# Kernel tuning notes

Measured on AMD Instinct MI355X. Metric: run time of the kernel, lower is better.

## Reference

```python
import jax, jax.numpy as jnp
import numpy as np

KAPPA = 8
TEMP = 200.0
EPS = 1e-15
N, E, D, T = 8192, 131072, 128, 8
P0, P1 = 512, 128
ZI = D - KAPPA  # non-kappa feature dims


def expmap0(u):
    # Poincare ball exp map at origin, c=1
    n = jnp.clip(jnp.linalg.norm(u, axis=-1, keepdims=True), EPS)
    return jnp.tanh(n) * u / n


def logmap0(y):
    # Poincare ball log map at origin, c=1 (clipped for numerical safety)
    n = jnp.clip(jnp.linalg.norm(y, axis=-1, keepdims=True), EPS)
    t = jnp.clip(n, EPS, 1.0 - 1e-5)
    return jnp.arctanh(t) * y / n


def setup_inputs() -> dict:
    key = jax.random.key(0)
    ks = jax.random.split(key, 8)
    g = lambda k, shp: jax.random.normal(k, shp, jnp.float32) / np.float32(np.sqrt(shp[0]))
    return {
        "x": 0.1 * jax.random.normal(ks[0], (N, D), jnp.float32),
        "y": jax.random.normal(ks[1], (T, N), jnp.float32),
        "We0": g(ks[2], (ZI, ZI)), "be0": jnp.zeros((ZI,), jnp.float32),
        "Ws0": g(ks[3], (D, P0)), "bs0": jnp.zeros((P0,), jnp.float32),
        "We1": g(ks[4], (ZI, ZI)), "be1": jnp.zeros((ZI,), jnp.float32),
        "Ws1": g(ks[5], (D, P1)), "bs1": jnp.zeros((P1,), jnp.float32),
        "adj": jax.random.randint(ks[6], (2, E), 0, N),
    }


def _embed_pool(z, agg, We, be, Ws, bs):
    # embed_pool: keep z0, message-pass zi; compute cluster scores s (hyperbolic head)
    z0, zi = z[:, :KAPPA], z[:, KAPPA:]
    zi = agg(zi @ We + be)
    s = expmap0(agg(z @ Ws + bs))
    z = jnp.concatenate([z0, zi], axis=-1)
    S = jax.nn.softmax(logmap0(s) * TEMP, axis=0)  # soft assignment over nodes
    return z, S


def reference(x, y, We0, be0, Ws0, bs0, We1, be1, Ws1, bs1, adj):
    n = x.shape[0]
    # dense adjacency at level 0 (as in the original renorm)
    A0 = jnp.zeros((n, n), x.dtype).at[adj[0], adj[1]].set(1.0)
    # sparse aggregation equivalent to A0 @ h
    agg0 = lambda h: jax.ops.segment_sum(h[adj[1]], adj[0], num_segments=n)

    # ---- level 0 ----
    z, S0 = _embed_pool(x, agg0, We0, be0, Ws0, bs0)
    x1 = jnp.einsum('ij,ik->jk', S0, z)        # [P0, D] pooled features
    y1 = jnp.einsum('ij,ki->kj', S0, y)        # [T, P0] pooled targets
    A1 = jnp.einsum('ji,jk,kl->il', S0, A0, S0)  # [P0, P0] coarsened adjacency
    loss_ent = jax.scipy.special.entr(S0).sum()

    # ---- level 1 (dense weighted adjacency, i.e. dense_to_coo(A1) round trip) ----
    agg1 = lambda h: A1 @ h
    z1, S1 = _embed_pool(x1, agg1, We1, be1, Ws1, bs1)
    x2 = jnp.einsum('ij,ik->jk', S1, z1)       # [P1, D]
    y2 = jnp.einsum('ij,ki->kj', S1, y1)       # [T, P1]
    loss_ent = loss_ent + jax.scipy.special.entr(S1).sum()

    z_r = jnp.concatenate([x, x1, x2], axis=0)   # [N+P0+P1, D]
    y_r = jnp.concatenate([y, y1, y2], axis=-1)  # [T, N+P0+P1]
    return z_r, y_r, loss_ent
```

## Files before the change

### kernel.cpp

```cpp
#include <hip/hip_runtime.h>
#include <hip/hip_bf16.h>

#define NC   8192
#define EC   131072
#define DC   128
#define TC   8
#define P0C  512
#define P1C  128
#define ZIC  120
#define NCAT 248
#define NW0  640
#define TEMPC 200.0f
#define ATANH_MAX 6.1053405f

typedef short short8 __attribute__((ext_vector_type(8)));
typedef float f32x4 __attribute__((ext_vector_type(4)));

__device__ inline unsigned short f2b(float f) {
  union { float f; unsigned u; } x; x.f = f;
  unsigned r = x.u + 0x7FFFu + ((x.u >> 16) & 1u);
  return (unsigned short)(r >> 16);
}
__device__ inline float b2f(unsigned short b) {
  union { unsigned u; float f; } x; x.u = ((unsigned)b) << 16; return x.f;
}

__global__ void k_prep(const float* __restrict__ Ws0, const float* __restrict__ We0,
                       const float* __restrict__ bs0, const float* __restrict__ be0,
                       const float* __restrict__ We1, const float* __restrict__ Ws1,
                       const float* __restrict__ be1, const float* __restrict__ bs1,
                       unsigned short* __restrict__ WcatHi, unsigned short* __restrict__ WcatLo,
                       float* __restrict__ bias0cat,
                       float* __restrict__ Bcat, float* __restrict__ biascat1)
{
  int idx = blockIdx.x * 256 + threadIdx.x;
  const int A = NW0 * DC;
  const int B = A + NW0;
  const int Cc = B + DC * NCAT;
  const int Dd = Cc + NCAT;
  if (idx < A) {
    int n = idx >> 7, k = idx & 127;
    float v;
    if (n < P0C) v = Ws0[(size_t)k * P0C + n];
    else {
      int nn = n - P0C;
      v = (nn < ZIC && k >= 8) ? We0[(size_t)(k - 8) * ZIC + nn] : 0.f;
    }
    unsigned short h = f2b(v);
    WcatHi[idx] = h; WcatLo[idx] = f2b(v - b2f(h));
  } else if (idx < B) {
    int n = idx - A;
    bias0cat[n] = (n < P0C) ? bs0[n] : ((n - P0C) < ZIC ? be0[n - P0C] : 0.f);
  } else if (idx < Cc) {
    int j = idx - B;
    int k = j / NCAT, n = j - k * NCAT;
    float v;
    if (n < ZIC) v = (k >= 8) ? We1[(size_t)(k - 8) * ZIC + n] : 0.f;
    else         v = Ws1[(size_t)k * P1C + (n - ZIC)];
    Bcat[j] = v;
  } else if (idx < Dd) {
    int n = idx - Cc;
    biascat1[n] = (n < ZIC) ? be1[n] : bs1[n - ZIC];
  }
}

__global__ __launch_bounds__(256) void k_mfma_hilo2(
    const unsigned short* __restrict__ Ahi, const unsigned short* __restrict__ Alo,
    const unsigned short* __restrict__ Bhi, const unsigned short* __restrict__ Blo,
    const float* __restrict__ bias, const float* __restrict__ degf,
    float* __restrict__ C0, float* __restrict__ C1)
{
  __shared__ unsigned short Ah[64][136], Al[64][136], Bh[64][136], Bl[64][136];
  const int bm = blockIdx.x * 64, bn = blockIdx.y * 64;
  const int tid = threadIdx.x;
  const int lane = tid & 63, wave = tid >> 6;
  const int lrow = lane & 15, lgrp = lane >> 4;
#pragma unroll
  for (int p = 0; p < 4; ++p) {
    int id = p * 256 + tid;
    int r = id >> 4, c = id & 15;
    *(uint4*)(&Ah[r][c * 8]) = *(const uint4*)(Ahi + (size_t)(bm + r) * 128 + c * 8);
    *(uint4*)(&Al[r][c * 8]) = *(const uint4*)(Alo + (size_t)(bm + r) * 128 + c * 8);
    *(uint4*)(&Bh[r][c * 8]) = *(const uint4*)(Bhi + (size_t)(bn + r) * 128 + c * 8);
    *(uint4*)(&Bl[r][c * 8]) = *(const uint4*)(Blo + (size_t)(bn + r) * 128 + c * 8);
  }
  __syncthreads();
  f32x4 acc[4];
#pragma unroll
  for (int nt = 0; nt < 4; ++nt) acc[nt] = (f32x4){0.f, 0.f, 0.f, 0.f};
#pragma unroll
  for (int kk = 0; kk < 4; ++kk) {
    short8 ah = *(const short8*)(&Ah[wave * 16 + lrow][kk * 32 + lgrp * 8]);
    short8 al = *(const short8*)(&Al[wave * 16 + lrow][kk * 32 + lgrp * 8]);
#pragma unroll
    for (int nt = 0; nt < 4; ++nt) {
      short8 bh = *(const short8*)(&Bh[nt * 16 + lrow][kk * 32 + lgrp * 8]);
      short8 bl = *(const short8*)(&Bl[nt * 16 + lrow][kk * 32 + lgrp * 8]);
      acc[nt] = __builtin_amdgcn_mfma_f32_16x16x32_bf16(ah, bh, acc[nt], 0, 0, 0);
      acc[nt] = __builtin_amdgcn_mfma_f32_16x16x32_bf16(ah, bl, acc[nt], 0, 0, 0);
      acc[nt] = __builtin_amdgcn_mfma_f32_16x16x32_bf16(al, bh, acc[nt], 0, 0, 0);
    }
  }
#pragma unroll
  for (int nt = 0; nt < 4; ++nt) {
    int n = bn + nt * 16 + lrow;
#pragma unroll
    for (int r = 0; r < 4; ++r) {
      int m = bm + wave * 16 + lgrp * 4 + r;
      float v = acc[nt][r] + degf[m] * bias[n];
      if (n < P0C) C0[(size_t)m * P0C + n] = v;
      else if (n - P0C < ZIC) C1[(size_t)m * DC + 8 + (n - P0C)] = v;
    }
  }
}

__global__ __launch_bounds__(256) void k_gemm_nn_part(
    const float* __restrict__ A, int lda,
    const float* __restrict__ B, int ldb,
    float* __restrict__ part,
    int M, int N, int K, int kchunk)
{
  __shared__ float As[16][65];
  __shared__ float Bs[16][65];
  int bm = blockIdx.x * 64, bn = blockIdx.y * 64;
  int z = blockIdx.z;
  int ks = z * kchunk, ke = min(K, ks + kchunk);
  int tid = threadIdx.x;
  int tm = (tid >> 4) << 2, tn = (tid & 15) << 2;
  float acc[4][4] = {};
  for (int k0 = ks; k0 < ke; k0 += 16) {
    for (int i = tid; i < 1024; i += 256) {
      int m = i >> 4, k = i & 15;
      float v = 0.f;
      if (bm + m < M && k0 + k < ke) v = A[(size_t)(bm + m) * lda + k0 + k];
      As[k][m] = v;
    }
    for (int i = tid; i < 1024; i += 256) {
      int k = i >> 6, n = i & 63;
      float v = 0.f;
      if (k0 + k < ke && bn + n < N) v = B[(size_t)(k0 + k) * ldb + bn + n];
      Bs[k][n] = v;
    }
    __syncthreads();
#pragma unroll
    for (int kk = 0; kk < 16; ++kk) {
      float a[4], b[4];
#pragma unroll
      for (int i = 0; i < 4; i++) a[i] = As[kk][tm + i];
#pragma unroll
      for (int j = 0; j < 4; j++) b[j] = Bs[kk][tn + j];
#pragma unroll
      for (int i = 0; i < 4; i++)
#pragma unroll
        for (int j = 0; j < 4; j++) acc[i][j] += a[i] * b[j];
    }
    __syncthreads();
  }
  size_t base = (size_t)z * M * N;
#pragma unroll
  for (int i = 0; i < 4; i++) {
    int m = bm + tm + i; if (m >= M) continue;
#pragma unroll
    for (int j = 0; j < 4; j++) {
      int n = bn + tn + j; if (n >= N) continue;
      part[base + (size_t)m * N + n] = acc[i][j];
    }
  }
}

__global__ void k_reduce_bias(const float* __restrict__ part,
                              const float* __restrict__ bias,
                              float* __restrict__ C, int nparts, int M, int N)
{
  int idx = blockIdx.x * 256 + threadIdx.x;
  if (idx >= M * N) return;
  int n = idx % N;
  float s = 0.f;
  for (int p = 0; p < nparts; ++p) s += part[(size_t)p * M * N + idx];
  if (bias) s += bias[n];
  C[idx] = s;
}

__global__ void k_reduce_stageB(const float* __restrict__ part,
                                const float* __restrict__ x1f,
                                float* __restrict__ z1, float* __restrict__ s1agg,
                                int nparts)
{
  int idx = blockIdx.x * 256 + threadIdx.x;
  const int MN = P0C * NCAT;
  if (idx < MN) {
    int m = idx / NCAT, n = idx - m * NCAT;
    float s = 0.f;
    for (int p = 0; p < nparts; ++p) s += part[(size_t)p * MN + idx];
    if (n < ZIC) z1[(size_t)m * DC + 8 + n] = s;
    else         s1agg[(size_t)m * P1C + (n - ZIC)] = s;
  } else if (idx < MN + P0C * 8) {
    int r = idx - MN; int m = r >> 3, c = r & 7;
    z1[(size_t)m * DC + c] = x1f[(size_t)m * DC + c];
  }
}

__global__ __launch_bounds__(256) void k_gemm_tn(
    const float* __restrict__ A, int lda,
    const float* __restrict__ B, int ldb,
    float* __restrict__ C, int ldc,
    int M, int N, int K, int kchunk)
{
  __shared__ float As[16][65];
  __shared__ float Bs[16][65];
  int bm = blockIdx.x * 64, bn = blockIdx.y * 64;
  int ks = blockIdx.z * kchunk;
  int ke = min(K, ks + kchunk);
  int tid = threadIdx.x;
  int tm = (tid >> 4) << 2, tn = (tid & 15) << 2;
  float acc[4][4] = {};
  for (int k0 = ks; k0 < ke; k0 += 16) {
    for (int i = tid; i < 1024; i += 256) {
      int k = i >> 6, m = i & 63;
      float v = 0.f;
      if (k0 + k < ke && bm + m < M) v = A[(size_t)(k0 + k) * lda + bm + m];
      As[k][m] = v;
    }
    for (int i = tid; i < 1024; i += 256) {
      int k = i >> 6, n = i & 63;
      float v = 0.f;
      if (k0 + k < ke && bn + n < N) v = B[(size_t)(k0 + k) * ldb + bn + n];
      Bs[k][n] = v;
    }
    __syncthreads();
#pragma unroll
    for (int kk = 0; kk < 16; ++kk) {
      float a[4], b[4];
#pragma unroll
      for (int i = 0; i < 4; i++) a[i] = As[kk][tm + i];
#pragma unroll
      for (int j = 0; j < 4; j++) b[j] = Bs[kk][tn + j];
#pragma unroll
      for (int i = 0; i < 4; i++)
#pragma unroll
        for (int j = 0; j < 4; j++) acc[i][j] += a[i] * b[j];
    }
    __syncthreads();
  }
#pragma unroll
  for (int i = 0; i < 4; i++) {
    int m = bm + tm + i; if (m >= M) continue;
#pragma unroll
    for (int j = 0; j < 4; j++) {
      int n = bn + tn + j; if (n >= N) continue;
      atomicAdd(&C[(size_t)m * ldc + n], acc[i][j]);
    }
  }
}

__global__ __launch_bounds__(256) void k_transpose_bf16(
    const float* __restrict__ src, int R, int C,
    unsigned short* __restrict__ dst)
{
  __shared__ float tile[64][65];
  int br = blockIdx.x * 64, bc = blockIdx.y * 64;
  for (int idx = threadIdx.x; idx < 4096; idx += 256) {
    int r = idx >> 6, c = idx & 63;
    tile[r][c] = src[(size_t)(br + r) * C + bc + c];
  }
  __syncthreads();
  for (int idx = threadIdx.x; idx < 4096; idx += 256) {
    int c = idx >> 6, r = idx & 63;
    dst[(size_t)(bc + c) * R + br + r] = f2b(tile[r][c]);
  }
}

__global__ __launch_bounds__(256) void k_transpose_b2b(
    const unsigned short* __restrict__ src, int R, int C,
    unsigned short* __restrict__ dst)
{
  __shared__ unsigned short tile[64][65];
  int br = blockIdx.x * 64, bc = blockIdx.y * 64;
  for (int idx = threadIdx.x; idx < 4096; idx += 256) {
    int r = idx >> 6, c = idx & 63;
    tile[r][c] = src[(size_t)(br + r) * C + bc + c];
  }
  __syncthreads();
  for (int idx = threadIdx.x; idx < 4096; idx += 256) {
    int c = idx >> 6, r = idx & 63;
    dst[(size_t)(bc + c) * R + br + r] = tile[r][c];
  }
}

__global__ __launch_bounds__(256) void k_nt_bf16(
    const unsigned short* __restrict__ At,
    const unsigned short* __restrict__ Bt,
    float* __restrict__ Cpart,
    int M, int N, int K, int kchunk)
{
  __shared__ unsigned short Alds[64][136];
  __shared__ unsigned short Blds[64][136];
  const int bm = blockIdx.x * 64, bn = blockIdx.y * 64;
  const int z = blockIdx.z;
  const int k_beg = z * kchunk, k_end = k_beg + kchunk;
  const int tid = threadIdx.x;
  const int lane = tid & 63, wave = tid >> 6;
  const int lrow = lane & 15, lgrp = lane >> 4;
  f32x4 acc[4];
#pragma unroll
  for (int nt = 0; nt < 4; ++nt) acc[nt] = (f32x4){0.f, 0.f, 0.f, 0.f};

  for (int k0 = k_beg; k0 < k_end; k0 += 128) {
#pragma unroll
    for (int p = 0; p < 4; ++p) {
      int id = p * 256 + tid;
      int r = id >> 4;
      int c = id & 15;
      *(uint4*)(&Alds[r][c * 8]) =
          *(const uint4*)(At + (size_t)(bm + r) * K + k0 + c * 8);
      *(uint4*)(&Blds[r][c * 8]) =
          *(const uint4*)(Bt + (size_t)(bn + r) * K + k0 + c * 8);
    }
    __syncthreads();
#pragma unroll
    for (int kk = 0; kk < 4; ++kk) {
      short8 af = *(const short8*)(&Alds[wave * 16 + lrow][kk * 32 + lgrp * 8]);
#pragma unroll
      for (int nt = 0; nt < 4; ++nt) {
        short8 bf = *(const short8*)(&Blds[nt * 16 + lrow][kk * 32 + lgrp * 8]);
        acc[nt] = __builtin_amdgcn_mfma_f32_16x16x32_bf16(af, bf, acc[nt], 0, 0, 0);
      }
    }
    __syncthreads();
  }
  size_t base = (size_t)z * M * N;
#pragma unroll
  for (int nt = 0; nt < 4; ++nt) {
    int n = bn + nt * 16 + lrow;
#pragma unroll
    for (int r = 0; r < 4; ++r) {
      int m = bm + wave * 16 + lgrp * 4 + r;
      Cpart[base + (size_t)m * N + n] = acc[nt][r];
    }
  }
}

__global__ void k_reduce_parts(const float* __restrict__ part, float* __restrict__ C,
                               int nparts, int sz)
{
  int idx = blockIdx.x * 256 + threadIdx.x;
  if (idx >= sz) return;
  float s = 0.f;
  for (int p = 0; p < nparts; ++p) s += part[(size_t)p * sz + idx];
  C[idx] = s;
}

__global__ void k_count(const int* __restrict__ adj, int* __restrict__ counts)
{
  int e = blockIdx.x * 256 + threadIdx.x;
  if (e < EC) atomicAdd(&counts[adj[e]], 1);
}

__global__ __launch_bounds__(1024) void k_scan(const int* __restrict__ counts,
                                               int* __restrict__ offsets,
                                               float* __restrict__ degf)
{
  __shared__ int tsum[1024];
  int tid = threadIdx.x;
  int base = tid * 8;
  int loc[8]; int s = 0;
#pragma unroll
  for (int i = 0; i < 8; i++) { loc[i] = s; s += counts[base + i]; }
  tsum[tid] = s;
  __syncthreads();
  for (int off = 1; off < 1024; off <<= 1) {
    int v = (tid >= off) ? tsum[tid - off] : 0;
    __syncthreads();
    tsum[tid] += v;
    __syncthreads();
  }
  int excl = (tid == 0) ? 0 : tsum[tid - 1];
#pragma unroll
  for (int i = 0; i < 8; i++) {
    offsets[base + i] = excl + loc[i];
    degf[base + i] = (float)counts[base + i];
  }
  if (tid == 1023) offsets[NC] = tsum[1023];
}

__global__ void k_scatter(const int* __restrict__ adj, const int* __restrict__ offsets,
                          int* __restrict__ fill, int* __restrict__ csr)
{
  int e = blockIdx.x * 256 + threadIdx.x;
  if (e < EC) {
    int d = adj[e], s = adj[EC + e];
    int p = atomicAdd(&fill[d], 1);
    csr[offsets[d] + p] = s;
  }
}

__global__ __launch_bounds__(128) void k_aggX(
    const int* __restrict__ offsets, const int* __restrict__ csr,
    const float* __restrict__ x,
    float* __restrict__ xa, float* __restrict__ z,
    unsigned short* __restrict__ hi, unsigned short* __restrict__ lo)
{
  int j = blockIdx.x;
  int beg = offsets[j], deg = offsets[j + 1] - beg;
  __shared__ int srcs[512];
  bool inl = (deg <= 512);
  if (inl) for (int i = threadIdx.x; i < deg; i += 128) srcs[i] = csr[beg + i];
  __syncthreads();
  int c = threadIdx.x;
  float acc = 0.f;
  if (inl) {
    int i = 0;
    for (; i + 4 <= deg; i += 4) {
      int s0 = srcs[i], s1 = srcs[i+1], s2 = srcs[i+2], s3 = srcs[i+3];
      float v0 = x[(size_t)s0 * DC + c], v1 = x[(size_t)s1 * DC + c];
      float v2 = x[(size_t)s2 * DC + c], v3 = x[(size_t)s3 * DC + c];
      acc += v0; acc += v1; acc += v2; acc += v3;
    }
    for (; i < deg; ++i) acc += x[(size_t)srcs[i] * DC + c];
  } else {
    for (int i = 0; i < deg; ++i) acc += x[(size_t)csr[beg + i] * DC + c];
  }
  xa[(size_t)j * DC + c] = acc;
  unsigned short h = f2b(acc);
  hi[(size_t)j * DC + c] = h;
  lo[(size_t)j * DC + c] = f2b(acc - b2f(h));
  if (c < 8) z[(size_t)j * DC + c] = x[(size_t)j * DC + c];
}

__global__ __launch_bounds__(256) void k_aggM_bf16(
    const int* __restrict__ offsets, const int* __restrict__ csr,
    const unsigned short* __restrict__ S0h, unsigned short* __restrict__ Mbh)
{
  int j = blockIdx.x;
  int beg = offsets[j], deg = offsets[j + 1] - beg;
  __shared__ int srcs[512];
  __shared__ int nv_s;
  bool inl = (deg <= 512);
  if (inl) for (int i = threadIdx.x; i < deg; i += 256) srcs[i] = csr[beg + i];
  __syncthreads();
  if (inl) {
    for (int t = threadIdx.x; t < deg; t += 256) {
      int v = srcs[t];
      for (int u = 0; u < t; ++u)
        if (csr[beg + u] == v) { srcs[t] = -1; break; }
    }
  }
  __syncthreads();
  if (threadIdx.x == 0) {
    int nv = 0;
    if (inl) {
      for (int i = 0; i < deg; i++) if (srcs[i] >= 0) srcs[nv++] = srcs[i];
    }
    nv_s = nv;
  }
  __syncthreads();
  int c2 = threadIdx.x;
  float a0 = 0.f, a1 = 0.f;
  if (inl) {
    int nv = nv_s;
    int i = 0;
    for (; i + 8 <= nv; i += 8) {
      ushort2 v0 = *(const ushort2*)(S0h + (size_t)srcs[i]   * P0C + c2 * 2);
      ushort2 v1 = *(const ushort2*)(S0h + (size_t)srcs[i+1] * P0C + c2 * 2);
      ushort2 v2 = *(const ushort2*)(S0h + (size_t)srcs[i+2] * P0C + c2 * 2);
      ushort2 v3 = *(const ushort2*)(S0h + (size_t)srcs[i+3] * P0C + c2 * 2);
      ushort2 v4 = *(const ushort2*)(S0h + (size_t)srcs[i+4] * P0C + c2 * 2);
      ushort2 v5 = *(const ushort2*)(S0h + (size_t)srcs[i+5] * P0C + c2 * 2);
      ushort2 v6 = *(const ushort2*)(S0h + (size_t)srcs[i+6] * P0C + c2 * 2);
      ushort2 v7 = *(const ushort2*)(S0h + (size_t)srcs[i+7] * P0C + c2 * 2);
      a0 += b2f(v0.x) + b2f(v1.x) + b2f(v2.x) + b2f(v3.x)
          + b2f(v4.x) + b2f(v5.x) + b2f(v6.x) + b2f(v7.x);
      a1 += b2f(v0.y) + b2f(v1.y) + b2f(v2.y) + b2f(v3.y)
          + b2f(v4.y) + b2f(v5.y) + b2f(v6.y) + b2f(v7.y);
    }
    for (; i < nv; ++i) {
      ushort2 v = *(const ushort2*)(S0h + (size_t)srcs[i] * P0C + c2 * 2);
      a0 += b2f(v.x); a1 += b2f(v.y);
    }
  } else {
    for (int i = 0; i < deg; i++) {
      int s = csr[beg + i];
      bool dup = false;
      for (int u = 0; u < i; u++) if (csr[beg + u] == s) { dup = true; break; }
      if (!dup) {
        ushort2 v = *(const ushort2*)(S0h + (size_t)s * P0C + c2 * 2);
        a0 += b2f(v.x); a1 += b2f(v.y);
      }
    }
  }
  ushort2 o2; o2.x = f2b(a0); o2.y = f2b(a1);
  *(ushort2*)(Mbh + (size_t)j * P0C + c2 * 2) = o2;
}

__global__ __launch_bounds__(256) void k_rowscale(const float* __restrict__ U, int cols,
                                                  float* __restrict__ rs)
{
  int r = blockIdx.x;
  const float* row = U + (size_t)r * cols;
  float ss = 0.f;
  for (int c = threadIdx.x; c < cols; c += 256) { float v = row[c]; ss += v * v; }
  for (int off = 32; off > 0; off >>= 1) ss += __shfl_down(ss, off);
  __shared__ float red[4];
  if ((threadIdx.x & 63) == 0) red[threadIdx.x >> 6] = ss;
  __syncthreads();
  if (threadIdx.x == 0) {
    float n = sqrtf(red[0] + red[1] + red[2] + red[3]);
    n = fmaxf(n, 1e-15f);
    rs[r] = TEMPC * fminf(n, ATANH_MAX) / n;
  }
}

__global__ __launch_bounds__(256) void k_smaxA(const float* __restrict__ U,
    const float* __restrict__ rs, float* __restrict__ pm, float* __restrict__ ps,
    int rows, int cols, int rpg)
{
  int lc = threadIdx.x & 63;
  int c = blockIdx.x * 64 + lc;
  int rl = threadIdx.x >> 6;
  int r0 = blockIdx.y * rpg, r1 = min(rows, r0 + rpg);
  float m = -1e30f, s = 0.f;
  for (int r = r0 + rl; r < r1; r += 4) {
    float l = rs[r] * U[(size_t)r * cols + c];
    if (l > m) { s = s * __expf(m - l) + 1.f; m = l; }
    else s += __expf(l - m);
  }
  __shared__ float sm[4][64], sv[4][64];
  sm[rl][lc] = m; sv[rl][lc] = s;
  __syncthreads();
  if (threadIdx.x < 64) {
    float mm = sm[0][threadIdx.x], s2 = sv[0][threadIdx.x];
    for (int q = 1; q < 4; q++) {
      float mq = sm[q][threadIdx.x], sq = sv[q][threadIdx.x];
      float mn = fmaxf(mm, mq);
      s2 = s2 * __expf(mm - mn) + sq * __expf(mq - mn);
      mm = mn;
    }
    pm[(size_t)blockIdx.y * cols + blockIdx.x * 64 + threadIdx.x] = mm;
    ps[(size_t)blockIdx.y * cols + blockIdx.x * 64 + threadIdx.x] = s2;
  }
}

__global__ void k_smaxB(const float* __restrict__ pm, const float* __restrict__ ps,
                        float* __restrict__ colm, float* __restrict__ colsum,
                        int ng, int cols)
{
  int c = blockIdx.x * blockDim.x + threadIdx.x;
  if (c >= cols) return;
  float m = -1e30f, s = 0.f;
  for (int g = 0; g < ng; g++) {
    float mg = pm[(size_t)g * cols + c], sg = ps[(size_t)g * cols + c];
    float mn = fmaxf(m, mg);
    s = s * __expf(m - mn) + sg * __expf(mg - mn);
    m = mn;
  }
  colm[c] = m; colsum[c] = s;
}

__global__ __launch_bounds__(256) void k_smaxC(const float* __restrict__ U,
    const float* __restrict__ rs, const float* __restrict__ colm,
    const float* __restrict__ colsum,
    unsigned short* __restrict__ Sh, unsigned short* __restrict__ ST,
    float* __restrict__ loss, int rows, int cols)
{
  __shared__ unsigned short tile[64][258];
  __shared__ float red[4];
  int lc = threadIdx.x & 63;
  int gc = blockIdx.x * 64 + lc;
  int rl = threadIdx.x >> 6;
  int r0 = blockIdx.y * 256;
  float m = colm[gc], inv = 1.f / colsum[gc];
  float h = 0.f;
  for (int rr = rl; rr < 256; rr += 4) {
    int r = r0 + rr;
    float l = rs[r] * U[(size_t)r * cols + gc];
    float p = __expf(l - m) * inv;
    unsigned short pb = f2b(p);
    Sh[(size_t)r * cols + gc] = pb;
    tile[lc][rr] = pb;
    if (p > 0.f) h -= p * __logf(p);
  }
  for (int off = 32; off > 0; off >>= 1) h += __shfl_down(h, off);
  if ((threadIdx.x & 63) == 0) red[threadIdx.x >> 6] = h;
  __syncthreads();
  if (threadIdx.x == 0) atomicAdd(loss, red[0] + red[1] + red[2] + red[3]);
  int gc0 = blockIdx.x * 64;
  for (int idx = threadIdx.x; idx < 64 * 256; idx += 256) {
    int col = idx >> 8, rr = idx & 255;
    ST[(size_t)(gc0 + col) * rows + r0 + rr] = tile[col][rr];
  }
}

__global__ __launch_bounds__(256) void k_smax_col(const float* __restrict__ U,
    const float* __restrict__ rs, float* __restrict__ S, float* __restrict__ loss,
    int rows, int cols)
{
  int c = blockIdx.x;
  int tid = threadIdx.x;
  int r0 = tid, r1 = tid + 256;
  float v0 = rs[r0] * U[(size_t)r0 * cols + c];
  float v1 = rs[r1] * U[(size_t)r1 * cols + c];
  float m = fmaxf(v0, v1);
  for (int off = 32; off > 0; off >>= 1) m = fmaxf(m, __shfl_xor(m, off));
  __shared__ float red[4];
  if ((tid & 63) == 0) red[tid >> 6] = m;
  __syncthreads();
  m = fmaxf(fmaxf(red[0], red[1]), fmaxf(red[2], red[3]));
  float e0 = __expf(v0 - m), e1 = __expf(v1 - m);
  float s = e0 + e1;
  for (int off = 32; off > 0; off >>= 1) s += __shfl_xor(s, off);
  __syncthreads();
  __shared__ float red2[4];
  if ((tid & 63) == 0) red2[tid >> 6] = s;
  __syncthreads();
  s = red2[0] + red2[1] + red2[2] + red2[3];
  float inv = 1.f / s;
  float p0 = e0 * inv, p1 = e1 * inv;
  S[(size_t)r0 * cols + c] = p0;
  S[(size_t)r1 * cols + c] = p1;
  float h = 0.f;
  if (p0 > 0.f) h -= p0 * __logf(p0);
  if (p1 > 0.f) h -= p1 * __logf(p1);
  for (int off = 32; off > 0; off >>= 1) h += __shfl_xor(h, off);
  __syncthreads();
  __shared__ float red3[4];
  if ((tid & 63) == 0) red3[tid >> 6] = h;
  __syncthreads();
  if (tid == 0) atomicAdd(loss, red3[0] + red3[1] + red3[2] + red3[3]);
}

__global__ __launch_bounds__(256) void k_yS_part(
    const float* __restrict__ Y, int ldy,
    const float* __restrict__ S, int ldS,
    float* __restrict__ part, int K, int C, int kchunk)
{
  int lc = threadIdx.x & 63;
  int c = blockIdx.x * 64 + lc;
  int rl = threadIdx.x >> 6;
  int r0 = blockIdx.y * kchunk, r1 = min(K, r0 + kchunk);
  float acc[8] = {};
  for (int r = r0 + rl; r < r1; r += 4) {
    float sv = S[(size_t)r * ldS + c];
#pragma unroll
    for (int t = 0; t < 8; t++) acc[t] += Y[(size_t)t * ldy + r] * sv;
  }
  __shared__ float red[4][8][64];
#pragma unroll
  for (int t = 0; t < 8; t++) red[rl][t][lc] = acc[t];
  __syncthreads();
  if (rl == 0) {
#pragma unroll
    for (int t = 0; t < 8; t++) {
      float v = red[0][t][lc] + red[1][t][lc] + red[2][t][lc] + red[3][t][lc];
      part[((size_t)blockIdx.y * 8 + t) * C + c] = v;
    }
  }
}

__global__ __launch_bounds__(256) void k_yS_part_b(
    const float* __restrict__ Y, int ldy,
    const unsigned short* __restrict__ S, int ldS,
    float* __restrict__ part, int K, int C, int kchunk)
{
  int lc = threadIdx.x & 63;
  int c = blockIdx.x * 64 + lc;
  int rl = threadIdx.x >> 6;
  int r0 = blockIdx.y * kchunk, r1 = min(K, r0 + kchunk);
  float acc[8] = {};
  for (int r = r0 + rl; r < r1; r += 4) {
    float sv = b2f(S[(size_t)r * ldS + c]);
#pragma unroll
    for (int t = 0; t < 8; t++) acc[t] += Y[(size_t)t * ldy + r] * sv;
  }
  __shared__ float red[4][8][64];
#pragma unroll
  for (int t = 0; t < 8; t++) red[rl][t][lc] = acc[t];
  __syncthreads();
  if (rl == 0) {
#pragma unroll
    for (int t = 0; t < 8; t++) {
      float v = red[0][t][lc] + red[1][t][lc] + red[2][t][lc] + red[3][t][lc];
      part[((size_t)blockIdx.y * 8 + t) * C + c] = v;
    }
  }
}

__global__ void k_yS_red(const float* __restrict__ part, float* __restrict__ outp,
                         int nparts, int sz)
{
  int idx = blockIdx.x * 256 + threadIdx.x;
  if (idx >= sz) return;
  float s = 0.f;
  for (int p = 0; p < nparts; ++p) s += part[(size_t)p * sz + idx];
  outp[idx] = s;
}

__global__ void k_emit_all(const float* __restrict__ x, const float* __restrict__ x1f,
                           const float* __restrict__ x2f, const float* __restrict__ y,
                           const float* __restrict__ y1f, const float* __restrict__ y2f,
                           const float* __restrict__ lossf, float* __restrict__ out,
                           int total)
{
  int idx = blockIdx.x * 256 + threadIdx.x;
  if (idx >= total) return;
  float v;
  if (idx < 1048576) v = x[idx];
  else if (idx < 1114112) v = x1f[idx - 1048576];
  else if (idx < 1130496) v = x2f[idx - 1114112];
  else if (idx < 1201152) {
    int r = idx - 1130496;
    int t = r / 8832, c = r - t * 8832;
    if (c < 8192) v = y[(size_t)t * 8192 + c];
    else if (c < 8704) v = y1f[t * 512 + (c - 8192)];
    else v = y2f[t * 128 + (c - 8704)];
  } else v = lossf[0];
  out[idx] = v;
}

extern "C" void kernel_launch(void* const* d_in, const int* in_sizes, int n_in,
                              void* d_out, int out_size, void* d_ws, size_t ws_size,
                              hipStream_t stream)
{
  (void)in_sizes; (void)n_in; (void)ws_size;
  const float* x   = (const float*)d_in[0];
  const float* y   = (const float*)d_in[1];
  const float* We0 = (const float*)d_in[2];
  const float* be0 = (const float*)d_in[3];
  const float* Ws0 = (const float*)d_in[4];
  const float* bs0 = (const float*)d_in[5];
  const float* We1 = (const float*)d_in[6];
  const float* be1 = (const float*)d_in[7];
  const float* Ws1 = (const float*)d_in[8];
  const float* bs1 = (const float*)d_in[9];
  const int*   adj = (const int*)d_in[10];
  float* out = (float*)d_out;

  float* ws = (float*)d_ws;
  size_t o = 0;
  auto alloc = [&](size_t n) { float* p = ws + o; o += n; return p; };
  float* xa    = alloc((size_t)NC * DC);
  float* sAgg  = alloc((size_t)NC * P0C);
  float* zbuf  = alloc((size_t)NC * DC);
  float* rsc   = alloc(NC);
  float* degf  = alloc(NC);
  float* pm    = alloc(32 * P0C);
  float* ps    = alloc(32 * P0C);
  float* colm  = alloc(P0C);
  float* colsum= alloc(P0C);
  float* s1agg = alloc((size_t)P0C * P1C);
  float* S1    = alloc((size_t)P0C * P1C);
  float* z1    = alloc((size_t)P0C * P1C);
  float* rs1   = alloc(P0C);
  float* x1f   = alloc((size_t)P0C * DC);
  float* A1    = alloc((size_t)P0C * P0C);
  unsigned short* S0T   = (unsigned short*)alloc((size_t)P0C * NC / 2);
  unsigned short* MbT   = (unsigned short*)alloc((size_t)P0C * NC / 2);
  unsigned short* zbufT = (unsigned short*)alloc((size_t)DC * NC / 2);
  unsigned short* S0h   = (unsigned short*)alloc((size_t)NC * P0C / 2);
  unsigned short* xaHi  = (unsigned short*)alloc((size_t)NC * DC / 2);
  unsigned short* xaLo  = (unsigned short*)alloc((size_t)NC * DC / 2);
  unsigned short* WcatHi= (unsigned short*)alloc((size_t)NW0 * DC / 2);
  unsigned short* WcatLo= (unsigned short*)alloc((size_t)NW0 * DC / 2);
  float* bias0cat = alloc(NW0);
  float* Bcat   = alloc((size_t)DC * NCAT);
  float* biascat1= alloc(NCAT);
  float* t1s1   = alloc((size_t)P0C * NCAT);
  float* partSA = alloc((size_t)4 * P0C * NCAT);
  float* partSB = alloc((size_t)8 * P0C * NCAT);
  float* partY1 = alloc((size_t)128 * TC * P0C);
  float* partY2 = alloc((size_t)8 * TC * P1C);
  float* x2f   = alloc((size_t)P1C * DC);
  float* y1f   = alloc((size_t)TC * P0C);
  float* y2f   = alloc((size_t)TC * P1C);
  float* lossf = alloc(1);
  size_t atomicFloats = (size_t)P1C*DC + (size_t)TC*P0C + (size_t)TC*P1C + 1;
  o = (o + 63) & ~(size_t)63;
  int* ibase   = (int*)(ws + o);
  int* counts  = ibase;
  int* fill    = ibase + NC;
  int* offsets = ibase + 2 * NC;
  int* csr     = ibase + 2 * NC + (NC + 1);

  unsigned short* Mbh = (unsigned short*)sAgg;
  float* partsA1 = sAgg + (size_t)2 * 1024 * 1024;
  float* partsX1 = zbuf;

  hipMemsetAsync(x2f, 0, atomicFloats * sizeof(float), stream);
  hipMemsetAsync(counts, 0, 2 * NC * sizeof(int), stream);

  k_count  <<<EC/256, 256, 0, stream>>>(adj, counts);
  k_scan   <<<1, 1024, 0, stream>>>(counts, offsets, degf);
  k_scatter<<<EC/256, 256, 0, stream>>>(adj, offsets, fill, csr);
  k_prep<<<(NW0*DC + NW0 + DC*NCAT + NCAT + 255)/256, 256, 0, stream>>>(
      Ws0, We0, bs0, be0, We1, Ws1, be1, bs1,
      WcatHi, WcatLo, bias0cat, Bcat, biascat1);

  k_aggX<<<NC, 128, 0, stream>>>(offsets, csr, x, xa, zbuf, xaHi, xaLo);
  k_mfma_hilo2<<<dim3(NC/64, NW0/64), 256, 0, stream>>>(xaHi, xaLo, WcatHi, WcatLo,
                                                        bias0cat, degf, sAgg, zbuf);
  k_transpose_bf16<<<dim3(NC/64, DC/64), 256, 0, stream>>>(zbuf, NC, DC, zbufT);

  k_rowscale<<<NC, 256, 0, stream>>>(sAgg, P0C, rsc);
  k_smaxA<<<dim3(P0C/64, 32), 256, 0, stream>>>(sAgg, rsc, pm, ps, NC, P0C, 256);
  k_smaxB<<<P0C/256, 256, 0, stream>>>(pm, ps, colm, colsum, 32, P0C);
  k_smaxC<<<dim3(P0C/64, 32), 256, 0, stream>>>(sAgg, rsc, colm, colsum, S0h, S0T, lossf, NC, P0C);

  k_aggM_bf16<<<NC, 256, 0, stream>>>(offsets, csr, S0h, Mbh);
  k_transpose_b2b<<<dim3(NC/64, P0C/64), 256, 0, stream>>>(Mbh, NC, P0C, MbT);

  k_nt_bf16<<<dim3(P0C/64, P0C/64, 8), 256, 0, stream>>>(S0T, MbT, partsA1, P0C, P0C, NC, 1024);
  k_reduce_parts<<<(P0C*P0C)/256, 256, 0, stream>>>(partsA1, A1, 8, P0C*P0C);
  k_nt_bf16<<<dim3(P0C/64, DC/64, 16), 256, 0, stream>>>(S0T, zbufT, partsX1, P0C, DC, NC, 512);
  k_reduce_parts<<<(P0C*DC)/256, 256, 0, stream>>>(partsX1, x1f, 16, P0C*DC);
  k_yS_part_b<<<dim3(P0C/64, 128), 256, 0, stream>>>(y, NC, S0h, P0C, partY1, NC, P0C, 64);
  k_yS_red<<<(TC*P0C + 255)/256, 256, 0, stream>>>(partY1, y1f, 128, TC*P0C);

  k_gemm_nn_part<<<dim3(P0C/64, 4, 4), 256, 0, stream>>>(x1f, DC, Bcat, NCAT, partSA, P0C, NCAT, DC, 32);
  k_reduce_bias<<<(P0C*NCAT + 255)/256, 256, 0, stream>>>(partSA, biascat1, t1s1, 4, P0C, NCAT);
  k_gemm_nn_part<<<dim3(P0C/64, 4, 8), 256, 0, stream>>>(A1, P0C, t1s1, NCAT, partSB, P0C, NCAT, P0C, 64);
  k_reduce_stageB<<<(P0C*NCAT + P0C*8 + 255)/256, 256, 0, stream>>>(partSB, x1f, z1, s1agg, 8);

  k_rowscale<<<P0C, 256, 0, stream>>>(s1agg, P1C, rs1);
  k_smax_col<<<P1C, 256, 0, stream>>>(s1agg, rs1, S1, lossf, P0C, P1C);
  k_gemm_tn<<<dim3(P1C/64, DC/64, 16), 256, 0, stream>>>(S1, P1C, z1, DC, x2f, DC, P1C, DC, P0C, 32);
  k_yS_part<<<dim3(P1C/64, 8), 256, 0, stream>>>(y1f, P0C, S1, P1C, partY2, P0C, P1C, 64);
  k_yS_red<<<(TC*P1C + 255)/256, 256, 0, stream>>>(partY2, y2f, 8, TC*P1C);

  k_emit_all<<<(out_size + 255)/256, 256, 0, stream>>>(x, x1f, x2f, y, y1f, y2f, lossf, out, out_size);
}
```

Baseline: 304.8 us.

## Fuse row-norm and bf16 transposed z output into level-0 MFMA epilogue

The level-0 MFMA GEMM epilogue now accumulates per-row sums of squares with shuffles and atomics, replacing the separate k_rowscale pass over the 8192x512 score matrix; a small kernel turns these into row scales. It also writes the message-passed z columns directly as transposed bf16, removing the fp32 zbuf and the k_transpose_bf16 kernel, and aggX writes the first 8 columns transposed. The fp32 xa store is dropped, and aggM now uses 512 threads with scalar bf16 loads instead of 256 threads with paired loads. The trade-off is extra atomics, strided 8-byte transposed stores, and a row norm summed in a different order.

```diff
diff --git a/kernel.cpp b/kernel.cpp
--- a/kernel.cpp
+++ b/kernel.cpp
@@ -68,7 +68,8 @@
     const unsigned short* __restrict__ Ahi, const unsigned short* __restrict__ Alo,
     const unsigned short* __restrict__ Bhi, const unsigned short* __restrict__ Blo,
     const float* __restrict__ bias, const float* __restrict__ degf,
-    float* __restrict__ C0, float* __restrict__ C1)
+    float* __restrict__ C0, unsigned short* __restrict__ zT,
+    float* __restrict__ rs_ss)
 {
   __shared__ unsigned short Ah[64][136], Al[64][136], Bh[64][136], Bl[64][136];
   const int bm = blockIdx.x * 64, bn = blockIdx.y * 64;
@@ -101,17 +102,58 @@
       acc[nt] = __builtin_amdgcn_mfma_f32_16x16x32_bf16(al, bh, acc[nt], 0, 0, 0);
     }
   }
-#pragma unroll
-  for (int nt = 0; nt < 4; ++nt) {
-    int n = bn + nt * 16 + lrow;
+  if (bn < P0C) {
+    float pr[4] = {0.f, 0.f, 0.f, 0.f};
+#pragma unroll
+    for (int nt = 0; nt < 4; ++nt) {
+      int n = bn + nt * 16 + lrow;
+#pragma unroll
+      for (int r = 0; r < 4; ++r) {
+        int m = bm + wave * 16 + lgrp * 4 + r;
+        float v = acc[nt][r] + degf[m] * bias[n];
+        C0[(size_t)m * P0C + n] = v;
+        pr[r] += v * v;
+      }
+    }
 #pragma unroll
     for (int r = 0; r < 4; ++r) {
-      int m = bm + wave * 16 + lgrp * 4 + r;
-      float v = acc[nt][r] + degf[m] * bias[n];
-      if (n < P0C) C0[(size_t)m * P0C + n] = v;
-      else if (n - P0C < ZIC) C1[(size_t)m * DC + 8 + (n - P0C)] = v;
-    }
-  }
+      float t = pr[r];
+      t += __shfl_down(t, 8, 16);
+      t += __shfl_down(t, 4, 16);
+      t += __shfl_down(t, 2, 16);
+      t += __shfl_down(t, 1, 16);
+      if (lrow == 0) {
+        int m = bm + wave * 16 + lgrp * 4 + r;
+        atomicAdd(&rs_ss[m], t);
+      }
+    }
+  } else {
+#pragma unroll
+    for (int nt = 0; nt < 4; ++nt) {
+      int n = bn + nt * 16 + lrow;
+      int col = n - P0C + 8;
+      if (col >= DC) continue;
+      int m0 = bm + wave * 16 + lgrp * 4;
+      ushort4 pk;
+      unsigned short* pp = (unsigned short*)&pk;
+#pragma unroll
+      for (int r = 0; r < 4; ++r) {
+        int m = m0 + r;
+        float v = acc[nt][r] + degf[m] * bias[n];
+        pp[r] = f2b(v);
+      }
+      *(ushort4*)(zT + (size_t)col * NC + m0) = pk;
+    }
+  }
+}
+
+__global__ void k_rs_final(const float* __restrict__ rs_ss, float* __restrict__ rs)
+{
+  int r = blockIdx.x * 256 + threadIdx.x;
+  if (r >= NC) return;
+  float n = sqrtf(rs_ss[r]);
+  n = fmaxf(n, 1e-15f);
+  rs[r] = TEMPC * fminf(n, ATANH_MAX) / n;
 }
 
 __global__ __launch_bounds__(256) void k_gemm_nn_part(
@@ -253,23 +295,6 @@
   }
 }
 
-__global__ __launch_bounds__(256) void k_transpose_bf16(
-    const float* __restrict__ src, int R, int C,
-    unsigned short* __restrict__ dst)
-{
-  __shared__ float tile[64][65];
-  int br = blockIdx.x * 64, bc = blockIdx.y * 64;
-  for (int idx = threadIdx.x; idx < 4096; idx += 256) {
-    int r = idx >> 6, c = idx & 63;
-    tile[r][c] = src[(size_t)(br + r) * C + bc + c];
-  }
-  __syncthreads();
-  for (int idx = threadIdx.x; idx < 4096; idx += 256) {
-    int c = idx >> 6, r = idx & 63;
-    dst[(size_t)(bc + c) * R + br + r] = f2b(tile[r][c]);
-  }
-}
-
 __global__ __launch_bounds__(256) void k_transpose_b2b(
     const unsigned short* __restrict__ src, int R, int C,
     unsigned short* __restrict__ dst)
@@ -397,8 +422,8 @@
 __global__ __launch_bounds__(128) void k_aggX(
     const int* __restrict__ offsets, const int* __restrict__ csr,
     const float* __restrict__ x,
-    float* __restrict__ xa, float* __restrict__ z,
-    unsigned short* __restrict__ hi, unsigned short* __restrict__ lo)
+    unsigned short* __restrict__ hi, unsigned short* __restrict__ lo,
+    unsigned short* __restrict__ zT)
 {
   int j = blockIdx.x;
   int beg = offsets[j], deg = offsets[j + 1] - beg;
@@ -420,14 +445,13 @@
   } else {
     for (int i = 0; i < deg; ++i) acc += x[(size_t)csr[beg + i] * DC + c];
   }
-  xa[(size_t)j * DC + c] = acc;
   unsigned short h = f2b(acc);
   hi[(size_t)j * DC + c] = h;
   lo[(size_t)j * DC + c] = f2b(acc - b2f(h));
-  if (c < 8) z[(size_t)j * DC + c] = x[(size_t)j * DC + c];
-}
-
-__global__ __launch_bounds__(256) void k_aggM_bf16(
+  if (c < 8) zT[(size_t)c * NC + j] = f2b(x[(size_t)j * DC + c]);
+}
+
+__global__ __launch_bounds__(512) void k_aggM_bf16(
     const int* __restrict__ offsets, const int* __restrict__ csr,
     const unsigned short* __restrict__ S0h, unsigned short* __restrict__ Mbh)
 {
@@ -436,10 +460,10 @@
   __shared__ int srcs[512];
   __shared__ int nv_s;
   bool inl = (deg <= 512);
-  if (inl) for (int i = threadIdx.x; i < deg; i += 256) srcs[i] = csr[beg + i];
+  if (inl) for (int i = threadIdx.x; i < deg; i += 512) srcs[i] = csr[beg + i];
   __syncthreads();
   if (inl) {
-    for (int t = threadIdx.x; t < deg; t += 256) {
+    for (int t = threadIdx.x; t < deg; t += 512) {
       int v = srcs[t];
       for (int u = 0; u < t; ++u)
         if (csr[beg + u] == v) { srcs[t] = -1; break; }
@@ -454,60 +478,32 @@
     nv_s = nv;
   }
   __syncthreads();
-  int c2 = threadIdx.x;
-  float a0 = 0.f, a1 = 0.f;
+  int c = threadIdx.x;
+  float a0 = 0.f;
   if (inl) {
     int nv = nv_s;
     int i = 0;
     for (; i + 8 <= nv; i += 8) {
-      ushort2 v0 = *(const ushort2*)(S0h + (size_t)srcs[i]   * P0C + c2 * 2);
-      ushort2 v1 = *(const ushort2*)(S0h + (size_t)srcs[i+1] * P0C + c2 * 2);
-      ushort2 v2 = *(const ushort2*)(S0h + (size_t)srcs[i+2] * P0C + c2 * 2);
-      ushort2 v3 = *(const ushort2*)(S0h + (size_t)srcs[i+3] * P0C + c2 * 2);
-      ushort2 v4 = *(const ushort2*)(S0h + (size_t)srcs[i+4] * P0C + c2 * 2);
-      ushort2 v5 = *(const ushort2*)(S0h + (size_t)srcs[i+5] * P0C + c2 * 2);
-      ushort2 v6 = *(const ushort2*)(S0h + (size_t)srcs[i+6] * P0C + c2 * 2);
-      ushort2 v7 = *(const ushort2*)(S0h + (size_t)srcs[i+7] * P0C + c2 * 2);
-      a0 += b2f(v0.x) + b2f(v1.x) + b2f(v2.x) + b2f(v3.x)
-          + b2f(v4.x) + b2f(v5.x) + b2f(v6.x) + b2f(v7.x);
-      a1 += b2f(v0.y) + b2f(v1.y) + b2f(v2.y) + b2f(v3.y)
-          + b2f(v4.y) + b2f(v5.y) + b2f(v6.y) + b2f(v7.y);
-    }
-    for (; i < nv; ++i) {
-      ushort2 v = *(const ushort2*)(S0h + (size_t)srcs[i] * P0C + c2 * 2);
-      a0 += b2f(v.x); a1 += b2f(v.y);
-    }
+      float v0 = b2f(S0h[(size_t)srcs[i]   * P0C + c]);
+      float v1 = b2f(S0h[(size_t)srcs[i+1] * P0C + c]);
+      float v2 = b2f(S0h[(size_t)srcs[i+2] * P0C + c]);
+      float v3 = b2f(S0h[(size_t)srcs[i+3] * P0C + c]);
+      float v4 = b2f(S0h[(size_t)srcs[i+4] * P0C + c]);
+      float v5 = b2f(S0h[(size_t)srcs[i+5] * P0C + c]);
+      float v6 = b2f(S0h[(size_t)srcs[i+6] * P0C + c]);
+      float v7 = b2f(S0h[(size_t)srcs[i+7] * P0C + c]);
+      a0 += v0 + v1 + v2 + v3 + v4 + v5 + v6 + v7;
+    }
+    for (; i < nv; ++i) a0 += b2f(S0h[(size_t)srcs[i] * P0C + c]);
   } else {
     for (int i = 0; i < deg; i++) {
       int s = csr[beg + i];
       bool dup = false;
       for (int u = 0; u < i; u++) if (csr[beg + u] == s) { dup = true; break; }
-      if (!dup) {
-        ushort2 v = *(const ushort2*)(S0h + (size_t)s * P0C + c2 * 2);
-        a0 += b2f(v.x); a1 += b2f(v.y);
-      }
-    }
-  }
-  ushort2 o2; o2.x = f2b(a0); o2.y = f2b(a1);
-  *(ushort2*)(Mbh + (size_t)j * P0C + c2 * 2) = o2;
-}
-
-__global__ __launch_bounds__(256) void k_rowscale(const float* __restrict__ U, int cols,
-                                                  float* __restrict__ rs)
-{
-  int r = blockIdx.x;
-  const float* row = U + (size_t)r * cols;
-  float ss = 0.f;
-  for (int c = threadIdx.x; c < cols; c += 256) { float v = row[c]; ss += v * v; }
-  for (int off = 32; off > 0; off >>= 1) ss += __shfl_down(ss, off);
-  __shared__ float red[4];
-  if ((threadIdx.x & 63) == 0) red[threadIdx.x >> 6] = ss;
-  __syncthreads();
-  if (threadIdx.x == 0) {
-    float n = sqrtf(red[0] + red[1] + red[2] + red[3]);
-    n = fmaxf(n, 1e-15f);
-    rs[r] = TEMPC * fminf(n, ATANH_MAX) / n;
-  }
+      if (!dup) a0 += b2f(S0h[(size_t)s * P0C + c]);
+    }
+  }
+  Mbh[(size_t)j * P0C + c] = f2b(a0);
 }
 
 __global__ __launch_bounds__(256) void k_smaxA(const float* __restrict__ U,
@@ -590,6 +586,24 @@
   }
 }
 
+__global__ __launch_bounds__(256) void k_rowscale(const float* __restrict__ U, int cols,
+                                                  float* __restrict__ rs)
+{
+  int r = blockIdx.x;
+  const float* row = U + (size_t)r * cols;
+  float ss = 0.f;
+  for (int c = threadIdx.x; c < cols; c += 256) { float v = row[c]; ss += v * v; }
+  for (int off = 32; off > 0; off >>= 1) ss += __shfl_down(ss, off);
+  __shared__ float red[4];
+  if ((threadIdx.x & 63) == 0) red[threadIdx.x >> 6] = ss;
+  __syncthreads();
+  if (threadIdx.x == 0) {
+    float n = sqrtf(red[0] + red[1] + red[2] + red[3]);
+    n = fmaxf(n, 1e-15f);
+    rs[r] = TEMPC * fminf(n, ATANH_MAX) / n;
+  }
+}
+
 __global__ __launch_bounds__(256) void k_smax_col(const float* __restrict__ U,
     const float* __restrict__ rs, float* __restrict__ S, float* __restrict__ loss,
     int rows, int cols)
@@ -737,7 +751,6 @@
   float* ws = (float*)d_ws;
   size_t o = 0;
   auto alloc = [&](size_t n) { float* p = ws + o; o += n; return p; };
-  float* xa    = alloc((size_t)NC * DC);
   float* sAgg  = alloc((size_t)NC * P0C);
   float* zbuf  = alloc((size_t)NC * DC);
   float* rsc   = alloc(NC);
@@ -768,11 +781,12 @@
   float* partSB = alloc((size_t)8 * P0C * NCAT);
   float* partY1 = alloc((size_t)128 * TC * P0C);
   float* partY2 = alloc((size_t)8 * TC * P1C);
+  float* rs_ss = alloc(NC);
   float* x2f   = alloc((size_t)P1C * DC);
   float* y1f   = alloc((size_t)TC * P0C);
   float* y2f   = alloc((size_t)TC * P1C);
   float* lossf = alloc(1);
-  size_t atomicFloats = (size_t)P1C*DC + (size_t)TC*P0C + (size_t)TC*P1C + 1;
+  size_t atomicFloats = (size_t)NC + (size_t)P1C*DC + (size_t)TC*P0C + (size_t)TC*P1C + 1;
   o = (o + 63) & ~(size_t)63;
   int* ibase   = (int*)(ws + o);
   int* counts  = ibase;
@@ -784,7 +798,7 @@
   float* partsA1 = sAgg + (size_t)2 * 1024 * 1024;
   float* partsX1 = zbuf;
 
-  hipMemsetAsync(x2f, 0, atomicFloats * sizeof(float), stream);
+  hipMemsetAsync(rs_ss, 0, atomicFloats * sizeof(float), stream);
   hipMemsetAsync(counts, 0, 2 * NC * sizeof(int), stream);
 
   k_count  <<<EC/256, 256, 0, stream>>>(adj, counts);
@@ -794,17 +808,16 @@
       Ws0, We0, bs0, be0, We1, Ws1, be1, bs1,
       WcatHi, WcatLo, bias0cat, Bcat, biascat1);
 
-  k_aggX<<<NC, 128, 0, stream>>>(offsets, csr, x, xa, zbuf, xaHi, xaLo);
+  k_aggX<<<NC, 128, 0, stream>>>(offsets, csr, x, xaHi, xaLo, zbufT);
   k_mfma_hilo2<<<dim3(NC/64, NW0/64), 256, 0, stream>>>(xaHi, xaLo, WcatHi, WcatLo,
-                                                        bias0cat, degf, sAgg, zbuf);
-  k_transpose_bf16<<<dim3(NC/64, DC/64), 256, 0, stream>>>(zbuf, NC, DC, zbufT);
-
-  k_rowscale<<<NC, 256, 0, stream>>>(sAgg, P0C, rsc);
+                                                        bias0cat, degf, sAgg, zbufT, rs_ss);
+  k_rs_final<<<NC/256, 256, 0, stream>>>(rs_ss, rsc);
+
   k_smaxA<<<dim3(P0C/64, 32), 256, 0, stream>>>(sAgg, rsc, pm, ps, NC, P0C, 256);
   k_smaxB<<<P0C/256, 256, 0, stream>>>(pm, ps, colm, colsum, 32, P0C);
   k_smaxC<<<dim3(P0C/64, 32), 256, 0, stream>>>(sAgg, rsc, colm, colsum, S0h, S0T, lossf, NC, P0C);
 
-  k_aggM_bf16<<<NC, 256, 0, stream>>>(offsets, csr, S0h, Mbh);
+  k_aggM_bf16<<<NC, 512, 0, stream>>>(offsets, csr, S0h, Mbh);
   k_transpose_b2b<<<dim3(NC/64, P0C/64), 256, 0, stream>>>(Mbh, NC, P0C, MbT);
 
   k_nt_bf16<<<dim3(P0C/64, P0C/64, 8), 256, 0, stream>>>(S0T, MbT, partsA1, P0C, P0C, NC, 1024);
```

Result: slower. 317.2 us (+4.0%).
